# Performance work log

Measured on AMD Instinct MI355X. Metric: run time of the kernel, lower is better.

Reference implementation:

```python
import jax, jax.numpy as jnp
import numpy as np

B, T, D = 2, 2048, 2048
NH, HD, R = 16, 128, 64
CQ, CKV = 1536, 512
WINDOW, CHUNK = 512, 256
MIN_SCALE, MAX_SCALE = 0.5, 2.0
ROPE_BASE = 500000.0
EPS = 1e-6


def setup_inputs() -> dict:
    key = jax.random.key(0)
    ks = jax.random.split(key, 12)
    w = lambda k, shape: (jax.random.normal(k, shape, jnp.float32) * 0.02)
    return {
        "x": jax.random.normal(ks[0], (B, T, D), jnp.float32),
        "uncertainty": jax.random.uniform(ks[1], (B, T), jnp.float32),
        "Wq_down": w(ks[2], (D, CQ)),
        "q_norm_w": jnp.ones((CQ,), jnp.float32),
        "Wq_up": w(ks[3], (CQ, NH * HD)),
        "Wq_rope": w(ks[4], (CQ, NH * R)),
        "Wkv_down": w(ks[5], (D, CKV)),
        "kv_norm_w": jnp.ones((CKV,), jnp.float32),
        "Wk_up": w(ks[6], (CKV, NH * HD)),
        "Wv_up": w(ks[7], (CKV, NH * HD)),
        "Wk_rope": w(ks[8], (D, NH * R)),
        "Wout": w(ks[9], (NH * HD, D)),
        "Wgate": w(ks[10], (D, 1)),
        "bgate": jnp.zeros((1,), jnp.float32),
    }


def rms_norm(x, w):
    return x * jax.lax.rsqrt(jnp.mean(x * x, axis=-1, keepdims=True) + EPS) * w


def epe_cos_sin(positions, uncertainty):
    # freq_idx = arange(r//2)*2/r ; theta = base**(-freq_idx)
    half = R // 2
    freq_idx = jnp.arange(half, dtype=jnp.float32) * 2.0 / R
    theta = ROPE_BASE ** (-freq_idx)                                  # [half]
    scale = MIN_SCALE + jnp.clip(uncertainty, 0.0, 1.0) * (MAX_SCALE - MIN_SCALE)  # [B,T]
    freqs = positions[None, :, None].astype(jnp.float32) * theta[None, None, :] * scale[:, :, None]
    freqs = freqs[:, :, None, :]                                      # [B,T,1,half]
    return jnp.cos(freqs), jnp.sin(freqs)


def apply_rope(x, cos, sin):
    # x: [B,T,nH,r]; rotate halves with per-(B,T) cos/sin broadcast over heads
    half = x.shape[-1] // 2
    x1, x2 = x[..., :half], x[..., half:]
    return jnp.concatenate([x1 * cos - x2 * sin, x2 * cos + x1 * sin], axis=-1)


def sliding_window_attn(Q, K, V, window, chunk):
    # Q,K: [B,nH,T,dk], V: [B,nH,T,dv]; chunked causal sliding-window
    b, nh, t, dk = Q.shape
    dv = V.shape[-1]
    half_w = window // 2
    n_chunks = t // chunk                    # T chosen multiple of chunk
    L = chunk + 2 * half_w
    Kp = jnp.pad(K, ((0, 0), (0, 0), (half_w, half_w), (0, 0)))
    Vp = jnp.pad(V, ((0, 0), (0, 0), (half_w, half_w), (0, 0)))
    starts = jnp.arange(n_chunks) * chunk
    idx = starts[:, None] + jnp.arange(L)[None, :]          # [nC,L] into padded axis
    Kw = Kp[:, :, idx]                                       # [B,nH,nC,L,dk]
    Vw = Vp[:, :, idx]                                       # [B,nH,nC,L,dv]
    Qc = Q.reshape(b, nh, n_chunks, chunk, dk)
    scores = jnp.einsum('bhcqd,bhckd->bhcqk', Qc, Kw) / jnp.sqrt(jnp.float32(dk))
    key_pos = idx - half_w                                   # actual key positions [nC,L]
    q_pos = starts[:, None] + jnp.arange(chunk)[None, :]     # [nC,chunk]
    mask = (key_pos[:, None, :] <= q_pos[:, :, None]) & (key_pos[:, None, :] >= 0)
    scores = jnp.where(mask[None, None], scores, -jnp.inf)
    p = jax.nn.softmax(scores, axis=-1)
    out = jnp.einsum('bhcqk,bhckd->bhcqd', p, Vw)
    return out.reshape(b, nh, t, dv)


def reference(x, uncertainty, Wq_down, q_norm_w, Wq_up, Wq_rope,
              Wkv_down, kv_norm_w, Wk_up, Wv_up, Wk_rope, Wout, Wgate, bgate):
    b, t, d = x.shape
    positions = jnp.arange(t)

    q_lat = rms_norm(x @ Wq_down, q_norm_w)                  # [B,T,CQ]
    q_c = (q_lat @ Wq_up).reshape(b, t, NH, HD)
    q_r = (q_lat @ Wq_rope).reshape(b, t, NH, R)
    kv_lat = rms_norm(x @ Wkv_down, kv_norm_w)               # [B,T,CKV]
    k_c = (kv_lat @ Wk_up).reshape(b, t, NH, HD)
    v = (kv_lat @ Wv_up).reshape(b, t, NH, HD)
    k_r = (x @ Wk_rope).reshape(b, t, NH, R)

    cos, sin = epe_cos_sin(positions, uncertainty)
    q_r = apply_rope(q_r, cos, sin)
    k_r = apply_rope(k_r, cos, sin)

    Q = jnp.concatenate([q_c, q_r], axis=-1).transpose(0, 2, 1, 3)   # [B,nH,T,HD+R]
    K = jnp.concatenate([k_c, k_r], axis=-1).transpose(0, 2, 1, 3)
    V = v.transpose(0, 2, 1, 3)                                       # [B,nH,T,HD]

    out_ar = sliding_window_attn(Q, K, V, WINDOW, CHUNK)

    # full bidirectional SDPA
    scale = 1.0 / jnp.sqrt(jnp.float32(HD + R))
    scores = jnp.einsum('bhqd,bhkd->bhqk', Q, K) * scale
    out_bidir = jnp.einsum('bhqk,bhkd->bhqd', jax.nn.softmax(scores, axis=-1), V)

    alpha = jax.nn.sigmoid((x @ Wgate + bgate)).squeeze(-1)           # [B,T]
    a = alpha[:, None, :, None]
    merged = a * out_bidir + (1.0 - a) * out_ar                       # [B,nH,T,HD]
    merged = merged.transpose(0, 2, 1, 3).reshape(b, t, NH * HD)
    return merged @ Wout, alpha
```

## Files before the change

kernel.cpp:

```cpp
#include <hip/hip_runtime.h>
#include <hip/hip_bf16.h>
#include <math.h>

typedef __hip_bfloat16 bf16;
using v8bf = __attribute__((ext_vector_type(8))) __bf16;
using v4f  = __attribute__((ext_vector_type(4))) float;
using f32x16 = __attribute__((ext_vector_type(16))) float;
using v4u = __attribute__((ext_vector_type(4))) unsigned;
using v4s = __attribute__((ext_vector_type(4))) short;
using v8s = __attribute__((ext_vector_type(8))) short;

#define T_SEQ 2048
#define DMODEL 2048
#define NHEADS 16
#define HDIM 128
#define RDIM 64

__device__ __forceinline__ short f2bfbits(float f) {
  bf16 h = __float2bfloat16(f);
  short s;
  __builtin_memcpy(&s, &h, 2);
  return s;
}

__device__ __forceinline__ unsigned pk2bf(float a, float b) {
  unsigned lo = (unsigned short)f2bfbits(a);
  unsigned hi = (unsigned short)f2bfbits(b);
  return lo | (hi << 16);
}

typedef const __attribute__((address_space(1))) unsigned gu32;
typedef __attribute__((address_space(3))) unsigned lu32;
__device__ __forceinline__ void gl_lds16(const void* g, void* l) {
  __builtin_amdgcn_global_load_lds((gu32*)g, (lu32*)l, 16, 0, 0);
}

__global__ void detect_k(const unsigned* __restrict__ x, int* __restrict__ flag) {
  __shared__ int cnt;
  if (threadIdx.x == 0) cnt = 0;
  __syncthreads();
  int c = 0;
#pragma unroll
  for (int i = 0; i < 4; i++) {
    unsigned w = x[threadIdx.x * 4 + i];
    unsigned e = (w >> 7) & 0xFFu;
    if (e < 97u || e > 157u) c++;
  }
  atomicAdd(&cnt, c);
  __syncthreads();
  if (threadIdx.x == 0) flag[0] = (cnt > 256) ? 1 : 0;
}

__global__ __launch_bounds__(256) void conv_all(const void* x_raw,
                                                const void* qnw_raw, const void* kvnw_raw,
                                                const void* wg_raw, const void* bg_raw,
                                                const void* unc_raw,
                                                bf16* xc, bf16* qnw, bf16* kvnw,
                                                bf16* wgc, bf16* bgc, float* uncf,
                                                const int* flag) {
  bool isf = (*flag != 0);
  if (blockIdx.x < 8192) {
    int i4 = blockIdx.x * 256 + threadIdx.x;
    v4s o;
    if (isf) {
      float4 v = ((const float4*)x_raw)[i4];
      o[0] = f2bfbits(v.x); o[1] = f2bfbits(v.y);
      o[2] = f2bfbits(v.z); o[3] = f2bfbits(v.w);
    } else {
      o = ((const v4s*)x_raw)[i4];
    }
    *reinterpret_cast<v4s*>(xc + (size_t)i4 * 4) = o;
  } else {
    int i = (blockIdx.x - 8192) * 256 + threadIdx.x;
    if (i < 1536) qnw[i] = isf ? __float2bfloat16(((const float*)qnw_raw)[i]) : ((const bf16*)qnw_raw)[i];
    else if (i < 2048) { int j = i - 1536; kvnw[j] = isf ? __float2bfloat16(((const float*)kvnw_raw)[j]) : ((const bf16*)kvnw_raw)[j]; }
    else if (i < 4096) { int j = i - 2048; wgc[j] = isf ? __float2bfloat16(((const float*)wg_raw)[j]) : ((const bf16*)wg_raw)[j]; }
    else if (i < 4097) bgc[0] = isf ? __float2bfloat16(((const float*)bg_raw)[0]) : ((const bf16*)bg_raw)[0];
    else if (i < 8193) { int j = i - 4097; uncf[j] = isf ? ((const float*)unc_raw)[j] : __bfloat162float(((const bf16*)unc_raw)[j]); }
  }
}

struct TP8 {
  const void* s[8];
  bf16* d[8];
  int rows[8];
  int cols[8];
  int pre[9];
};

__global__ __launch_bounds__(256) void transpose_all(TP8 jobs, const int* __restrict__ flag) {
  __shared__ bf16 tile[32][33];
  int bid = blockIdx.x;
  int w = 0;
#pragma unroll
  for (int k = 0; k < 7; k++) if (bid >= jobs.pre[k + 1]) w = k + 1;
  int lt = bid - jobs.pre[w];
  int rows = jobs.rows[w], cols = jobs.cols[w];
  int tpr = cols >> 5;
  int by = (lt / tpr) << 5, bx = (lt % tpr) << 5;
  const void* src = jobs.s[w];
  bf16* dst = jobs.d[w];
  int tx = threadIdx.x & 31, ty = threadIdx.x >> 5;
  bool isf = (*flag != 0);
#pragma unroll
  for (int i = 0; i < 32; i += 8) {
    size_t idx = (size_t)(by + ty + i) * cols + bx + tx;
    tile[ty + i][tx] = isf ? __float2bfloat16(((const float*)src)[idx])
                           : ((const bf16*)src)[idx];
  }
  __syncthreads();
#pragma unroll
  for (int i = 0; i < 32; i += 8)
    dst[(size_t)(bx + ty + i) * rows + by + tx] = tile[tx][ty + i];
}

__global__ __launch_bounds__(256) void transpose_str(const bf16* __restrict__ src,
                                                     bf16* __restrict__ dst,
                                                     int srcStride, int dstStride) {
  __shared__ bf16 tile[32][33];
  int bx = blockIdx.x * 32, by = blockIdx.y * 32;
  int tx = threadIdx.x & 31, ty = threadIdx.x >> 5;
#pragma unroll
  for (int i = 0; i < 32; i += 8)
    tile[ty + i][tx] = src[(size_t)(by + ty + i) * srcStride + bx + tx];
  __syncthreads();
#pragma unroll
  for (int i = 0; i < 32; i += 8)
    dst[(size_t)(bx + ty + i) * dstStride + by + tx] = tile[tx][ty + i];
}

__global__ __launch_bounds__(256) void gemm_tn(const bf16* __restrict__ A,
                                               const bf16* __restrict__ BT,
                                               bf16* __restrict__ Cb,
                                               int M, int N, int K,
                                               const int* __restrict__ oflag,
                                               void* __restrict__ dvout) {
  __shared__ __align__(16) short lsa[128 * 32];
  __shared__ __align__(16) short lsb[128 * 32];
  const int m0 = blockIdx.y * 128, n0 = blockIdx.x * 128;
  const int tid = threadIdx.x;
  const int w = tid >> 6, lane = tid & 63, quad = lane >> 4, l16 = lane & 15;
  const int wm = (w >> 1) * 64, wn = (w & 1) * 64;
  const int srow = ((lane >> 5) & 1) * 8 + (lane & 7);
  const int skq  = (lane >> 3) & 3;
  const int r0 = w * 2, r1 = w * 2 + 1;
  const bf16* Ab0 = A  + (size_t)(m0 + r0 * 16 + srow) * K + skq * 8;
  const bf16* Ab1 = A  + (size_t)(m0 + r1 * 16 + srow) * K + skq * 8;
  const bf16* Bb0 = BT + (size_t)(n0 + r0 * 16 + srow) * K + skq * 8;
  const bf16* Bb1 = BT + (size_t)(n0 + r1 * 16 + srow) * K + skq * 8;
  short* la0 = &lsa[r0 * 512];
  short* la1 = &lsa[r1 * 512];
  short* lb0 = &lsb[r0 * 512];
  short* lb1 = &lsb[r1 * 512];

  v4f acc[4][4];
#pragma unroll
  for (int i = 0; i < 4; i++)
#pragma unroll
    for (int j = 0; j < 4; j++) acc[i][j] = (v4f){0.f, 0.f, 0.f, 0.f};

  for (int kb = 0; kb < K; kb += 32) {
    __syncthreads();
    gl_lds16(Ab0 + kb, la0);
    gl_lds16(Ab1 + kb, la1);
    gl_lds16(Bb0 + kb, lb0);
    gl_lds16(Bb1 + kb, lb1);
    __syncthreads();

    v8bf af[4], bfr[4];
#pragma unroll
    for (int i = 0; i < 4; i++) {
      int row = wm + i * 16 + l16;
      af[i] = *reinterpret_cast<const v8bf*>(
          &lsa[((row >> 3) << 8) + (quad << 6) + ((row & 7) << 3)]);
    }
#pragma unroll
    for (int j = 0; j < 4; j++) {
      int row = wn + j * 16 + l16;
      bfr[j] = *reinterpret_cast<const v8bf*>(
          &lsb[((row >> 3) << 8) + (quad << 6) + ((row & 7) << 3)]);
    }
#pragma unroll
    for (int i = 0; i < 4; i++)
#pragma unroll
      for (int j = 0; j < 4; j++)
        acc[i][j] = __builtin_amdgcn_mfma_f32_16x16x32_bf16(af[i], bfr[j], acc[i][j], 0, 0, 0);
  }
  const bool isf = dvout && (*oflag != 0);
#pragma unroll
  for (int i = 0; i < 4; i++)
#pragma unroll
    for (int j = 0; j < 4; j++)
#pragma unroll
      for (int r = 0; r < 4; r++) {
        int row = m0 + wm + i * 16 + quad * 4 + r;
        int col = n0 + wn + j * 16 + l16;
        float vv = acc[i][j][r];
        size_t idx = (size_t)row * N + col;
        if (dvout) {
          if (isf) ((float*)dvout)[idx] = vv;
          else     ((bf16*)dvout)[idx] = __float2bfloat16(vv);
        } else {
          Cb[idx] = __float2bfloat16(vv);
        }
      }
}

__global__ __launch_bounds__(256) void rmsnorm_both(const bf16* __restrict__ xproj,
                                                    const bf16* __restrict__ qnw,
                                                    const bf16* __restrict__ kvnw,
                                                    bf16* __restrict__ q_lat,
                                                    bf16* __restrict__ kv_lat) {
  int bid = blockIdx.x, tid = threadIdx.x;
  bool isq = bid < 4096;
  int row = isq ? bid : bid - 4096;
  int C = isq ? 1536 : 512;
  const bf16* r = xproj + (size_t)row * 3072 + (isq ? 0 : 1536);
  const bf16* w = isq ? qnw : kvnw;
  bf16* o = (isq ? q_lat : kv_lat) + (size_t)row * C;
  float s = 0.f;
  for (int i = tid; i < C; i += 256) { float v = __bfloat162float(r[i]); s += v * v; }
#pragma unroll
  for (int m = 32; m; m >>= 1) s += __shfl_xor(s, m);
  __shared__ float red[4];
  if ((tid & 63) == 0) red[tid >> 6] = s;
  __syncthreads();
  float tot = red[0] + red[1] + red[2] + red[3];
  float rs = rsqrtf(tot / (float)C + 1e-6f);
  for (int i = tid; i < C; i += 256)
    o[i] = __float2bfloat16(__bfloat162float(r[i]) * rs * __bfloat162float(w[i]));
}

__global__ __launch_bounds__(256) void rope_gate(bf16* __restrict__ qcr,
                                                 bf16* __restrict__ xproj,
                                                 const float* __restrict__ unc,
                                                 const bf16* __restrict__ x,
                                                 const bf16* __restrict__ wg,
                                                 const bf16* __restrict__ bg,
                                                 float* __restrict__ af,
                                                 void* __restrict__ dout,
                                                 const int* __restrict__ flag) {
  __shared__ float red[4];
  int tid = threadIdx.x;
  if (blockIdx.x < 8192) {
    int idx = blockIdx.x * 256 + tid;
    int j = idx & 31, h = (idx >> 5) & 15, bt = idx >> 9;
    int t = bt & (T_SEQ - 1);
    float u = unc[bt];
    u = fminf(fmaxf(u, 0.f), 1.f);
    float scale = 0.5f + 1.5f * u;
    float theta = expf(-(float)j * (1.f / 32.f) * logf(500000.f));
    float f = (float)t * theta * scale;
    float c = cosf(f), s = sinf(f);
    size_t base = (size_t)bt * 3072 + 2048 + h * RDIM + j;
    {
      float x1 = __bfloat162float(qcr[base]), x2 = __bfloat162float(qcr[base + 32]);
      qcr[base]      = __float2bfloat16(x1 * c - x2 * s);
      qcr[base + 32] = __float2bfloat16(x2 * c + x1 * s);
    }
    {
      float x1 = __bfloat162float(xproj[base]), x2 = __bfloat162float(xproj[base + 32]);
      xproj[base]      = __float2bfloat16(x1 * c - x2 * s);
      xproj[base + 32] = __float2bfloat16(x2 * c + x1 * s);
    }
  } else {
    int row = blockIdx.x - 8192;
    const bf16* xr = x + (size_t)row * DMODEL;
    float s = 0.f;
    for (int i = tid; i < DMODEL; i += 256)
      s += __bfloat162float(xr[i]) * __bfloat162float(wg[i]);
#pragma unroll
    for (int m = 32; m; m >>= 1) s += __shfl_xor(s, m);
    if ((tid & 63) == 0) red[tid >> 6] = s;
    __syncthreads();
    if (tid == 0) {
      float tot = red[0] + red[1] + red[2] + red[3] + __bfloat162float(bg[0]);
      float a = 1.f / (1.f + expf(-tot));
      af[row] = a;
      size_t oi = (size_t)8388608 + row;
      if (*flag) ((float*)dout)[oi] = a;
      else       ((bf16*)dout)[oi] = __float2bfloat16(a);
    }
  }
}

__global__ __launch_bounds__(512, 2) void attn_f(const bf16* __restrict__ qcr,
                                                 const bf16* __restrict__ kcv,
                                                 const bf16* __restrict__ xproj,
                                                 const bf16* __restrict__ vt,
                                                 const float* __restrict__ alphaF,
                                                 bf16* __restrict__ out) {
  constexpr int LDK = 200;
  constexpr int LDV = 72;
  __shared__ __align__(16) short sh[64 * LDK + 128 * LDV];
  short* lk  = sh;
  short* lvt = sh + 64 * LDK;

  const int f_ = blockIdx.x;
  const int xcd = f_ & 7, g_ = f_ >> 3;
  const int qt = g_ & 7;
  const int p_ = xcd + 8 * (g_ >> 3);
  const int h = p_ & 15, b = p_ >> 4;

  const int qs = qt * 256;
  const int tid = threadIdx.x;
  const int w = tid >> 6, lane = tid & 63;
  const int l5 = lane & 31, h8 = lane >> 5;
  const int q0 = qs + w * 32;
  const int myq = q0 + l5;

  v8bf qf[12];
  {
    const bf16* qcb = qcr + ((size_t)b * T_SEQ + myq) * 3072 + h * HDIM;
#pragma unroll
    for (int ks = 0; ks < 8; ks++)
      qf[ks] = *reinterpret_cast<const v8bf*>(qcb + ks * 16 + h8 * 8);
    const bf16* qrb = qcr + ((size_t)b * T_SEQ + myq) * 3072 + 2048 + h * RDIM;
#pragma unroll
    for (int ks = 0; ks < 4; ks++)
      qf[8 + ks] = *reinterpret_cast<const v8bf*>(qrb + ks * 16 + h8 * 8);
  }

  float l_sum = 0.f, l_snap = 0.f;
  f32x16 oacc[4], snap[4];
#pragma unroll
  for (int nd = 0; nd < 4; nd++)
#pragma unroll
    for (int r = 0; r < 16; r++) { oacc[nd][r] = 0.f; snap[nd][r] = 0.f; }

  const float a_q = alphaF[b * T_SEQ + myq];
  const float sc = 0.07216878364870323f;

  const int klo  = (qt > 0) ? (qs - 256) : 0;
  const int kb_d = qs + (w >> 1) * 64;

  const int koc0 = (tid >> 4) * 4096 + (tid & 15) * 8;
  const int ldc0 = (tid >> 4) * LDK  + (tid & 15) * 8;
  const int kor0 = (tid >> 3) * 3072 + (tid & 7) * 8;
  const int ldr0 = (tid >> 3) * LDK + 128 + (tid & 7) * 8;
  const int kov0 = (tid >> 3) * 4096 + (tid & 7) * 8;
  const int ldv0 = (tid >> 3) * LDV  + (tid & 7) * 8;
  const bf16* kc_base = kcv   + (size_t)b * T_SEQ * 4096 + h * HDIM;
  const bf16* kr_base = xproj + (size_t)b * T_SEQ * 3072 + 2048 + h * RDIM;
  const bf16* v_base  = vt    + (size_t)h * HDIM * (2 * T_SEQ) + b * T_SEQ;

  v4u rc[2], rr1, rv[2];
  auto issue = [&](int kb) {
    const bf16* pc = kc_base + (size_t)kb * 4096;
    const bf16* pr = kr_base + (size_t)kb * 3072;
    const bf16* pv = v_base + kb;
#pragma unroll
    for (int i = 0; i < 2; i++) rc[i] = *reinterpret_cast<const v4u*>(pc + koc0 + i * 131072);
    rr1 = *reinterpret_cast<const v4u*>(pr + kor0);
#pragma unroll
    for (int i = 0; i < 2; i++) rv[i] = *reinterpret_cast<const v4u*>(pv + kov0 + i * 262144);
  };

  auto qk = [&](int j) -> f32x16 {
    f32x16 s;
#pragma unroll
    for (int r = 0; r < 16; r++) s[r] = 0.f;
#pragma unroll
    for (int ks = 0; ks < 12; ks++) {
      v8bf kf = *reinterpret_cast<const v8bf*>(&lk[(j * 32 + l5) * LDK + ks * 16 + h8 * 8]);
      s = __builtin_amdgcn_mfma_f32_32x32x16_bf16(kf, qf[ks], s, 0, 0, 0);
    }
    return s;
  };
  auto pack8 = [&](const float* p) -> v8bf {
    unsigned Y0 = pk2bf(p[0], p[1]);
    unsigned Y1 = pk2bf(p[2], p[3]);
    unsigned Y2 = pk2bf(p[4], p[5]);
    unsigned Y3 = pk2bf(p[6], p[7]);
    asm volatile("v_permlane32_swap_b32 %0, %1" : "+v"(Y0), "+v"(Y2));
    asm volatile("v_permlane32_swap_b32 %0, %1" : "+v"(Y1), "+v"(Y3));
    v4u t; t.x = Y0; t.y = Y1; t.z = Y2; t.w = Y3;
    return __builtin_bit_cast(v8bf, t);
  };
  auto pvj = [&](int j, const v8bf* pf) {
#pragma unroll
    for (int ck = 0; ck < 2; ck++)
#pragma unroll
      for (int nd = 0; nd < 4; nd++) {
        v8bf vf = *reinterpret_cast<const v8bf*>(&lvt[(nd * 32 + l5) * LDV + (j * 2 + ck) * 16 + h8 * 8]);
        oacc[nd] = __builtin_amdgcn_mfma_f32_32x32x16_bf16(vf, pf[ck], oacc[nd], 0, 0, 0);
      }
  };
  auto plainpass = [&](int j) {
    f32x16 s = qk(j);
    v8bf pf[2];
#pragma unroll
    for (int cc = 0; cc < 2; cc++) {
      float p[8];
#pragma unroll
      for (int r8 = 0; r8 < 8; r8++) {
        float e = __expf(s[cc * 8 + r8] * sc);
        p[r8] = e;
        l_sum += e;
      }
      pf[cc] = pack8(p);
    }
    pvj(j, pf);
  };
  auto maskpass = [&](int j, int kb, bool upper) {
    f32x16 s = qk(j);
    v8bf pf[2];
#pragma unroll
    for (int cc = 0; cc < 2; cc++) {
      float p[8];
#pragma unroll
      for (int r8 = 0; r8 < 8; r8++) {
        int r = cc * 8 + r8;
        int kk = kb + j * 32 + (r & 3) + 8 * (r >> 2) + 4 * h8;
        float e = __expf(s[r] * sc);
        bool keep = upper ? (kk > myq) : (kk <= myq);
        e = keep ? e : 0.f;
        p[r8] = e;
        l_sum += e;
      }
      pf[cc] = pack8(p);
    }
    pvj(j, pf);
  };

  issue(0);

  for (int kb = 0; kb < T_SEQ; kb += 64) {
    __syncthreads();
#pragma unroll
    for (int i = 0; i < 2; i++) *reinterpret_cast<v4u*>(&lk[ldc0 + i * 32 * LDK]) = rc[i];
    *reinterpret_cast<v4u*>(&lk[ldr0]) = rr1;
#pragma unroll
    for (int i = 0; i < 2; i++) *reinterpret_cast<v4u*>(&lvt[ldv0 + i * 64 * LDV]) = rv[i];
    if (kb + 64 < T_SEQ) issue(kb + 64);
    __syncthreads();

    if (kb == klo) {
#pragma unroll
      for (int nd = 0; nd < 4; nd++) snap[nd] = oacc[nd];
      l_snap = l_sum;
    }

    __builtin_amdgcn_s_setprio(1);
    if (kb != kb_d) {
      plainpass(0);
      plainpass(1);
    } else {
      maskpass(0, kb, false);
      maskpass(1, kb, false);
      {
        float lar_h = l_sum - l_snap;
        float lar = lar_h + __shfl_xor(lar_h, 32);
        float sAR = (1.f - a_q) / lar;
#pragma unroll
        for (int nd = 0; nd < 4; nd++)
#pragma unroll
          for (int r = 0; r < 16; r++)
            snap[nd][r] = (oacc[nd][r] - snap[nd][r]) * sAR;
      }
      maskpass(0, kb, true);
      maskpass(1, kb, true);
    }
    __builtin_amdgcn_s_setprio(0);
  }

  l_sum += __shfl_xor(l_sum, 32);
  float inv = a_q / l_sum;

  __syncthreads();
#pragma unroll
  for (int ph = 0; ph < 2; ph++) {
    bool act = (w >> 2) == ph;
    short* tile = sh + (w & 3) * (32 * 136);
    if (act) {
#pragma unroll
      for (int nd = 0; nd < 4; nd++)
#pragma unroll
        for (int rg = 0; rg < 4; rg++) {
          v4s pk;
#pragma unroll
          for (int i = 0; i < 4; i++) {
            float val = oacc[nd][rg * 4 + i] * inv + snap[nd][rg * 4 + i];
            pk[i] = f2bfbits(val);
          }
          *reinterpret_cast<v4s*>(&tile[l5 * 136 + nd * 32 + rg * 8 + h8 * 4]) = pk;
        }
    }
    __syncthreads();
    if (act) {
#pragma unroll
      for (int i = 0; i < 8; i++) {
        int r = i * 4 + (lane >> 4);
        int q2 = q0 + r;
        int dcol = (lane & 15) * 8;
        v8s mv = *reinterpret_cast<const v8s*>(&tile[r * 136 + dcol]);
        size_t gbase = ((size_t)b * T_SEQ + q2) * DMODEL + h * HDIM + dcol;
        *reinterpret_cast<v8s*>((void*)(out + gbase)) = mv;
      }
    }
    __syncthreads();
  }
}

extern "C" void kernel_launch(void* const* d_in, const int* in_sizes, int n_in,
                              void* d_out, int out_size, void* d_ws, size_t ws_size,
                              hipStream_t stream) {
  const void* x_raw    = d_in[0];
  const void* unc_raw  = d_in[1];
  const void* Wqd_raw  = d_in[2];
  const void* qnw_raw  = d_in[3];
  const void* Wqu_raw  = d_in[4];
  const void* Wqr_raw  = d_in[5];
  const void* Wkvd_raw = d_in[6];
  const void* kvnw_raw = d_in[7];
  const void* Wku_raw  = d_in[8];
  const void* Wvu_raw  = d_in[9];
  const void* Wkr_raw  = d_in[10];
  const void* Wo_raw   = d_in[11];
  const void* Wg_raw   = d_in[12];
  const void* bg_raw   = d_in[13];

  char* ws = (char*)d_ws;
  size_t off = 0;
  auto alloc = [&](size_t bytes) -> void* {
    char* p = ws + off;
    off += (bytes + 255) & ~(size_t)255;
    return p;
  };
  int*  flag   = (int*)alloc(256);
  bf16* xc     = (bf16*)alloc((size_t)4096 * 2048 * 2);
  float* uncf  = (float*)alloc((size_t)4096 * 4);
  bf16* qnw    = (bf16*)alloc(1536 * 2);
  bf16* kvnw   = (bf16*)alloc(512 * 2);
  bf16* wgc    = (bf16*)alloc(2048 * 2);
  bf16* bgc    = (bf16*)alloc(256);
  bf16* BT1    = (bf16*)alloc((size_t)3072 * 2048 * 2);
  bf16* BT2    = (bf16*)alloc((size_t)3072 * 1536 * 2);
  bf16* BT3    = (bf16*)alloc((size_t)4096 * 512 * 2);
  bf16* WoT    = (bf16*)alloc((size_t)2048 * 2048 * 2);
  bf16* xproj  = (bf16*)alloc((size_t)4096 * 3072 * 2);
  bf16* q_lat  = (bf16*)alloc((size_t)4096 * 1536 * 2);
  bf16* kv_lat = (bf16*)alloc((size_t)4096 * 512 * 2);
  bf16* qcr    = (bf16*)alloc((size_t)4096 * 3072 * 2);
  bf16* kcv    = (bf16*)alloc((size_t)4096 * 4096 * 2);
  bf16* vT     = (bf16*)alloc((size_t)4096 * 2048 * 2);
  bf16* attno  = (bf16*)alloc((size_t)4096 * 2048 * 2);
  float* alphaF= (float*)alloc((size_t)4096 * 4);

  detect_k<<<1, 256, 0, stream>>>((const unsigned*)x_raw, flag);

  conv_all<<<8225, 256, 0, stream>>>(x_raw, qnw_raw, kvnw_raw, Wg_raw, bg_raw, unc_raw,
                                     xc, qnw, kvnw, wgc, bgc, uncf, flag);

  TP8 jobs;
  const void* srcs[8] = {Wqd_raw, Wkvd_raw, Wkr_raw, Wqu_raw, Wqr_raw, Wku_raw, Wvu_raw, Wo_raw};
  bf16* dsts[8] = {BT1, BT1 + (size_t)1536 * 2048, BT1 + (size_t)2048 * 2048,
                   BT2, BT2 + (size_t)2048 * 1536,
                   BT3, BT3 + (size_t)2048 * 512, WoT};
  int rws[8] = {2048, 2048, 2048, 1536, 1536, 512, 512, 2048};
  int cls[8] = {1536, 512, 1024, 2048, 1024, 2048, 2048, 2048};
  int acc_t = 0;
  for (int i = 0; i < 8; i++) {
    jobs.s[i] = srcs[i]; jobs.d[i] = dsts[i];
    jobs.rows[i] = rws[i]; jobs.cols[i] = cls[i];
    jobs.pre[i] = acc_t;
    acc_t += (rws[i] / 32) * (cls[i] / 32);
  }
  jobs.pre[8] = acc_t;
  transpose_all<<<acc_t, 256, 0, stream>>>(jobs, flag);

  auto gemmb = [&](const bf16* A, const bf16* BT, bf16* C, int M, int N, int K) {
    gemm_tn<<<dim3(N / 128, M / 128), 256, 0, stream>>>(A, BT, C, M, N, K, nullptr, nullptr);
  };

  gemmb(xc, BT1, xproj, 4096, 3072, 2048);
  rmsnorm_both<<<8192, 256, 0, stream>>>(xproj, qnw, kvnw, q_lat, kv_lat);
  gemmb(q_lat, BT2, qcr, 4096, 3072, 1536);
  gemmb(kv_lat, BT3, kcv, 4096, 4096, 512);

  transpose_str<<<dim3(64, 128), 256, 0, stream>>>(kcv + 2048, vT, 4096, 4096);

  rope_gate<<<12288, 256, 0, stream>>>(qcr, xproj, uncf, xc, wgc, bgc, alphaF, d_out, flag);

  attn_f<<<256, 512, 0, stream>>>(qcr, kcv, xproj, vT, alphaF, attno);

  gemm_tn<<<dim3(16, 32), 256, 0, stream>>>(attno, WoT, nullptr, 4096, 2048, 2048, flag, d_out);

  (void)in_sizes; (void)n_in; (void)out_size; (void)ws_size;
}
```

Measured before the change: 640.9 us.

## Replace GEMM with 256x256 double-buffered 8-wave pipelined MFMA kernel

Replaces the 128x128 single-buffered GEMM with a 512-thread kernel that computes 256x256 tiles over K=64 steps. Global-to-LDS loads are double-buffered and issued in quarter phases interleaved with MFMA work, gated by explicit vmcnt waits and barriers. An XOR swizzle on the LDS layout avoids bank conflicts, and s_setprio raises priority around the MFMA bursts. The aim is to hide memory latency and raise reuse per tile. In exchange, the larger tiles give fewer blocks (e.g. 12x16 for the first GEMM), which may underfill the CUs, and the hand-tuned wait counts are fragile.

New measurement: 606.4 us. 1.06x faster.

```diff
diff --git a/kernel.cpp b/kernel.cpp
--- a/kernel.cpp
+++ b/kernel.cpp
@@ -33,6 +33,11 @@
 typedef __attribute__((address_space(3))) unsigned lu32;
 __device__ __forceinline__ void gl_lds16(const void* g, void* l) {
   __builtin_amdgcn_global_load_lds((gu32*)g, (lu32*)l, 16, 0, 0);
+}
+
+template <int N>
+__device__ __forceinline__ void vwn() {
+  asm volatile("s_waitcnt vmcnt(%0)" :: "n"(N) : "memory");
 }
 
 __global__ void detect_k(const unsigned* __restrict__ x, int* __restrict__ flag) {
@@ -129,81 +134,134 @@
     dst[(size_t)(bx + ty + i) * dstStride + by + tx] = tile[tx][ty + i];
 }
 
-__global__ __launch_bounds__(256) void gemm_tn(const bf16* __restrict__ A,
-                                               const bf16* __restrict__ BT,
-                                               bf16* __restrict__ Cb,
-                                               int M, int N, int K,
-                                               const int* __restrict__ oflag,
-                                               void* __restrict__ dvout) {
-  __shared__ __align__(16) short lsa[128 * 32];
-  __shared__ __align__(16) short lsb[128 * 32];
-  const int m0 = blockIdx.y * 128, n0 = blockIdx.x * 128;
+__global__ __launch_bounds__(512, 2) void gemm8(const bf16* __restrict__ A,
+                                                const bf16* __restrict__ BT,
+                                                bf16* __restrict__ Cb,
+                                                int M, int N, int K,
+                                                const int* __restrict__ oflag,
+                                                void* __restrict__ dvout) {
+  __shared__ __align__(16) short lds[2][2][16384];
+  const int m0 = blockIdx.y * 256, n0 = blockIdx.x * 256;
   const int tid = threadIdx.x;
-  const int w = tid >> 6, lane = tid & 63, quad = lane >> 4, l16 = lane & 15;
-  const int wm = (w >> 1) * 64, wn = (w & 1) * 64;
-  const int srow = ((lane >> 5) & 1) * 8 + (lane & 7);
-  const int skq  = (lane >> 3) & 3;
-  const int r0 = w * 2, r1 = w * 2 + 1;
-  const bf16* Ab0 = A  + (size_t)(m0 + r0 * 16 + srow) * K + skq * 8;
-  const bf16* Ab1 = A  + (size_t)(m0 + r1 * 16 + srow) * K + skq * 8;
-  const bf16* Bb0 = BT + (size_t)(n0 + r0 * 16 + srow) * K + skq * 8;
-  const bf16* Bb1 = BT + (size_t)(n0 + r1 * 16 + srow) * K + skq * 8;
-  short* la0 = &lsa[r0 * 512];
-  short* la1 = &lsa[r1 * 512];
-  short* lb0 = &lsb[r0 * 512];
-  short* lb1 = &lsb[r1 * 512];
-
-  v4f acc[4][4];
-#pragma unroll
-  for (int i = 0; i < 4; i++)
-#pragma unroll
-    for (int j = 0; j < 4; j++) acc[i][j] = (v4f){0.f, 0.f, 0.f, 0.f};
-
-  for (int kb = 0; kb < K; kb += 32) {
-    __syncthreads();
-    gl_lds16(Ab0 + kb, la0);
-    gl_lds16(Ab1 + kb, la1);
-    gl_lds16(Bb0 + kb, lb0);
-    gl_lds16(Bb1 + kb, lb1);
-    __syncthreads();
-
-    v8bf af[4], bfr[4];
-#pragma unroll
-    for (int i = 0; i < 4; i++) {
-      int row = wm + i * 16 + l16;
-      af[i] = *reinterpret_cast<const v8bf*>(
-          &lsa[((row >> 3) << 8) + (quad << 6) + ((row & 7) << 3)]);
-    }
-#pragma unroll
-    for (int j = 0; j < 4; j++) {
-      int row = wn + j * 16 + l16;
-      bfr[j] = *reinterpret_cast<const v8bf*>(
-          &lsb[((row >> 3) << 8) + (quad << 6) + ((row & 7) << 3)]);
-    }
-#pragma unroll
-    for (int i = 0; i < 4; i++)
-#pragma unroll
-      for (int j = 0; j < 4; j++)
-        acc[i][j] = __builtin_amdgcn_mfma_f32_16x16x32_bf16(af[i], bfr[j], acc[i][j], 0, 0, 0);
-  }
+  const int w = tid >> 6, lane = tid & 63;
+  const int quad4 = lane >> 4, l16 = lane & 15;
+  const int wmq = (w >> 1) * 32;
+  const int wnq = (w & 1) * 64;
+
+  v4f acc[4][2][4];
+#pragma unroll
+  for (int qi = 0; qi < 4; qi++)
+#pragma unroll
+    for (int mf = 0; mf < 2; mf++)
+#pragma unroll
+      for (int nf = 0; nf < 4; nf++) acc[qi][mf][nf] = (v4f){0.f, 0.f, 0.f, 0.f};
+
+  auto stage_half = [&](int sp, int kb, int sbuf) {
+    const int mat = (sp == 0 || sp == 3) ? 0 : 1;
+    const int half = (sp >= 2) ? 1 : 0;
+    const bf16* base = mat ? BT : A;
+    const int rbase = (mat ? n0 : m0) + half * 128 + w * 16;
+#pragma unroll
+    for (int i = 0; i < 2; i++) {
+      int lrow = half * 128 + w * 16 + i * 8;
+      short* dst = &lds[sbuf][mat][lrow * 64];
+      int rl = i * 8 + (lane >> 3);
+      int grow = rbase + i * 8 + (lane >> 3);
+      int cb = ((lane & 7) * 16) ^ ((rl & 12) << 3);
+      const bf16* src = base + (size_t)grow * K + kb + (cb >> 1);
+      gl_lds16(src, dst);
+    }
+  };
+
+#define GEMM8_PHASE(BUF, PH, STAGE_STMT, WAIT_STMT) do {                          \
+    constexpr int qm_ = (PH) >> 1, qn_ = (PH) & 1;                                \
+    v8bf a_[2][2], b_[2][4];                                                      \
+    _Pragma("unroll")                                                             \
+    for (int ks = 0; ks < 2; ks++) {                                              \
+      _Pragma("unroll")                                                           \
+      for (int mf = 0; mf < 2; mf++) {                                            \
+        int r_ = qm_ * 128 + wmq + mf * 16 + l16;                                 \
+        int c_ = (ks * 64 + quad4 * 16) ^ ((r_ & 12) << 3);                       \
+        a_[ks][mf] = *reinterpret_cast<const v8bf*>(                              \
+            (const char*)&lds[BUF][0][0] + r_ * 128 + c_);                        \
+      }                                                                           \
+      _Pragma("unroll")                                                           \
+      for (int nf = 0; nf < 4; nf++) {                                            \
+        int r_ = qn_ * 128 + wnq + nf * 16 + l16;                                 \
+        int c_ = (ks * 64 + quad4 * 16) ^ ((r_ & 12) << 3);                       \
+        b_[ks][nf] = *reinterpret_cast<const v8bf*>(                              \
+            (const char*)&lds[BUF][1][0] + r_ * 128 + c_);                        \
+      }                                                                           \
+    }                                                                             \
+    STAGE_STMT;                                                                   \
+    WAIT_STMT;                                                                    \
+    __builtin_amdgcn_s_barrier();                                                 \
+    __builtin_amdgcn_s_setprio(1);                                                \
+    _Pragma("unroll")                                                             \
+    for (int ks = 0; ks < 2; ks++)                                                \
+      _Pragma("unroll")                                                           \
+      for (int mf = 0; mf < 2; mf++)                                              \
+        _Pragma("unroll")                                                         \
+        for (int nf = 0; nf < 4; nf++)                                            \
+          acc[qm_ * 2 + qn_][mf][nf] = __builtin_amdgcn_mfma_f32_16x16x32_bf16(   \
+              a_[ks][mf], b_[ks][nf], acc[qm_ * 2 + qn_][mf][nf], 0, 0, 0);       \
+    __builtin_amdgcn_s_setprio(0);                                                \
+    __builtin_amdgcn_s_barrier();                                                 \
+  } while (0)
+
+  const int T = K >> 6;
+
+#pragma unroll
+  for (int sp = 0; sp < 4; sp++) stage_half(sp, 0, 0);
+#pragma unroll
+  for (int sp = 0; sp < 4; sp++) stage_half(sp, 64, 1);
+  vwn<12>();
+  __builtin_amdgcn_s_barrier();
+
+  GEMM8_PHASE(0, 0, (void)0, vwn<10>());
+  GEMM8_PHASE(0, 1, (void)0, vwn<8>());
+  GEMM8_PHASE(0, 2, (void)0, (void)0);
+  GEMM8_PHASE(0, 3, (void)0, vwn<4>());
+
+  for (int t = 1; t <= T - 2; t++) {
+    const int buf = t & 1, sbuf = buf ^ 1, kbn = (t + 1) << 6;
+    GEMM8_PHASE(buf, 0, stage_half(0, kbn, sbuf), vwn<4>());
+    GEMM8_PHASE(buf, 1, stage_half(1, kbn, sbuf), vwn<4>());
+    GEMM8_PHASE(buf, 2, stage_half(2, kbn, sbuf), (void)0);
+    GEMM8_PHASE(buf, 3, stage_half(3, kbn, sbuf), vwn<4>());
+  }
+
+  {
+    const int buf = (T - 1) & 1;
+    GEMM8_PHASE(buf, 0, (void)0, vwn<2>());
+    GEMM8_PHASE(buf, 1, (void)0, vwn<0>());
+    GEMM8_PHASE(buf, 2, (void)0, (void)0);
+    GEMM8_PHASE(buf, 3, (void)0, (void)0);
+  }
+#undef GEMM8_PHASE
+
   const bool isf = dvout && (*oflag != 0);
 #pragma unroll
-  for (int i = 0; i < 4; i++)
-#pragma unroll
-    for (int j = 0; j < 4; j++)
-#pragma unroll
-      for (int r = 0; r < 4; r++) {
-        int row = m0 + wm + i * 16 + quad * 4 + r;
-        int col = n0 + wn + j * 16 + l16;
-        float vv = acc[i][j][r];
-        size_t idx = (size_t)row * N + col;
-        if (dvout) {
-          if (isf) ((float*)dvout)[idx] = vv;
-          else     ((bf16*)dvout)[idx] = __float2bfloat16(vv);
-        } else {
-          Cb[idx] = __float2bfloat16(vv);
+  for (int qi = 0; qi < 4; qi++) {
+    const int qm = qi >> 1, qn = qi & 1;
+#pragma unroll
+    for (int mf = 0; mf < 2; mf++)
+#pragma unroll
+      for (int nf = 0; nf < 4; nf++)
+#pragma unroll
+        for (int r = 0; r < 4; r++) {
+          int row = m0 + qm * 128 + wmq + mf * 16 + quad4 * 4 + r;
+          int col = n0 + qn * 128 + wnq + nf * 16 + l16;
+          float vv = acc[qi][mf][nf][r];
+          size_t idx = (size_t)row * N + col;
+          if (dvout) {
+            if (isf) ((float*)dvout)[idx] = vv;
+            else     ((bf16*)dvout)[idx] = __float2bfloat16(vv);
+          } else {
+            Cb[idx] = __float2bfloat16(vv);
+          }
         }
-      }
+  }
 }
 
 __global__ __launch_bounds__(256) void rmsnorm_both(const bf16* __restrict__ xproj,
@@ -569,14 +627,15 @@
   jobs.pre[8] = acc_t;
   transpose_all<<<acc_t, 256, 0, stream>>>(jobs, flag);
 
-  auto gemmb = [&](const bf16* A, const bf16* BT, bf16* C, int M, int N, int K) {
-    gemm_tn<<<dim3(N / 128, M / 128), 256, 0, stream>>>(A, BT, C, M, N, K, nullptr, nullptr);
-  };
-
-  gemmb(xc, BT1, xproj, 4096, 3072, 2048);
+  auto gemm8b = [&](const bf16* A, const bf16* BT, bf16* C, int M, int N, int K,
+                    const int* oflag, void* dvout) {
+    gemm8<<<dim3(N / 256, M / 256), 512, 0, stream>>>(A, BT, C, M, N, K, oflag, dvout);
+  };
+
+  gemm8b(xc, BT1, xproj, 4096, 3072, 2048, nullptr, nullptr);
   rmsnorm_both<<<8192, 256, 0, stream>>>(xproj, qnw, kvnw, q_lat, kv_lat);
-  gemmb(q_lat, BT2, qcr, 4096, 3072, 1536);
-  gemmb(kv_lat, BT3, kcv, 4096, 4096, 512);
+  gemm8b(q_lat, BT2, qcr, 4096, 3072, 1536, nullptr, nullptr);
+  gemm8b(kv_lat, BT3, kcv, 4096, 4096, 512, nullptr, nullptr);
 
   transpose_str<<<dim3(64, 128), 256, 0, stream>>>(kcv + 2048, vT, 4096, 4096);
 
@@ -584,7 +643,7 @@
 
   attn_f<<<256, 512, 0, stream>>>(qcr, kcv, xproj, vT, alphaF, attno);
 
-  gemm_tn<<<dim3(16, 32), 256, 0, stream>>>(attno, WoT, nullptr, 4096, 2048, 2048, flag, d_out);
+  gemm8b(attno, WoT, nullptr, 4096, 2048, 2048, flag, d_out);
 
   (void)in_sizes; (void)n_in; (void)out_size; (void)ws_size;
 }
```
